# Kernel tuning notes

Measured on AMD Instinct MI355X. Metric: run time of the kernel, lower is better.

Reference implementation:

```python
import jax, jax.numpy as jnp
import numpy as np

H = 64          # hidden_size
L = 5           # num_layers
D_IN = 45       # input_size
D_LAT = 128     # latent dim
D_OUT = 4       # output classes


def _lstm_layer(x, W_ih, W_hh, b):
    """One LSTM layer, batch_first input x:[B,T,D]. PyTorch gate order i,f,g,o."""
    # Precompute input contribution for all timesteps: [B,T,4H]
    xg = jnp.einsum('btd,gd->btg', x, W_ih) + b
    xg = jnp.swapaxes(xg, 0, 1)  # [T,B,4H] for scan
    B = x.shape[0]
    h0 = jnp.zeros((B, H), x.dtype)
    c0 = jnp.zeros((B, H), x.dtype)

    def step(carry, xt):
        h, c = carry
        g = xt + h @ W_hh.T                      # [B,4H]
        i, f, gg, o = jnp.split(g, 4, axis=-1)
        c = jax.nn.sigmoid(f) * c + jax.nn.sigmoid(i) * jnp.tanh(gg)
        h = jax.nn.sigmoid(o) * jnp.tanh(c)
        return (h, c), h

    (_, _), hs = jax.lax.scan(step, (h0, c0), xg)  # hs: [T,B,H]
    return jnp.swapaxes(hs, 0, 1)                  # [B,T,H]


def setup_inputs() -> dict:
    key = jax.random.key(0)
    ks = jax.random.split(key, 12)
    s = 1.0 / np.sqrt(H)  # PyTorch LSTM init scale
    x = jax.random.normal(ks[0], (256, 2048, D_IN), jnp.float32)
    W_ih0 = jax.random.uniform(ks[1], (4 * H, D_IN), jnp.float32, -s, s)
    W_ih_rest = jax.random.uniform(ks[2], (L - 1, 4 * H, H), jnp.float32, -s, s)
    W_hh = jax.random.uniform(ks[3], (L, 4 * H, H), jnp.float32, -s, s)
    b_ih = jax.random.uniform(ks[4], (L, 4 * H), jnp.float32, -s, s)
    b_hh = jax.random.uniform(ks[5], (L, 4 * H), jnp.float32, -s, s)
    Wl = jax.random.normal(ks[6], (D_LAT, H), jnp.float32) * 0.05
    bl = jnp.zeros((D_LAT,), jnp.float32)
    Wo = jax.random.normal(ks[7], (D_OUT, D_LAT), jnp.float32) * 0.05
    bo = jnp.zeros((D_OUT,), jnp.float32)
    return dict(x=x, W_ih0=W_ih0, W_ih_rest=W_ih_rest, W_hh=W_hh,
                b_ih=b_ih, b_hh=b_hh, Wl=Wl, bl=bl, Wo=Wo, bo=bo)


def reference(x, W_ih0, W_ih_rest, W_hh, b_ih, b_hh, Wl, bl, Wo, bo):
    # 5-layer LSTM (eval mode: inter-layer dropout inactive)
    h = _lstm_layer(x, W_ih0, W_hh[0], b_ih[0] + b_hh[0])
    for l in range(1, L):
        h = _lstm_layer(h, W_ih_rest[l - 1], W_hh[l], b_ih[l] + b_hh[l])
    last = h[:, -1, :]                                  # [B,H]
    features = jax.nn.gelu(last @ Wl.T + bl, approximate=False)  # [B,128]
    out = jax.nn.relu(features @ Wo.T + bo)             # [B,4]
    return out, features
```

## Files before the change

### kernel.cpp

```cpp
#include <hip/hip_runtime.h>
#include <hip/hip_fp16.h>
#include <math.h>

#define NCH   1024
#define KMAX  1034
#define HID   64
typedef unsigned int uint;
typedef __attribute__((ext_vector_type(2))) _Float16 h2t;

__device__ __forceinline__ float sigmoid_(float x){ return 1.0f/(1.0f+__expf(-x)); }
__device__ __forceinline__ float tanh_(float x){ float e=__expf(2.0f*x); return 1.0f-2.0f/(e+1.0f); }

__device__ __forceinline__ float fdot2_(uint w, uint h, float acc){
#if __has_builtin(__builtin_amdgcn_fdot2)
    return __builtin_amdgcn_fdot2(__builtin_bit_cast(h2t,w), __builtin_bit_cast(h2t,h), acc, false);
#else
    __half2 wv = *reinterpret_cast<const __half2*>(&w);
    __half2 hv = *reinterpret_cast<const __half2*>(&h);
    float2 wf = __half22float2(wv), hf = __half22float2(hv);
    return fmaf(wf.x, hf.x, fmaf(wf.y, hf.y, acc));
#endif
}
__device__ __forceinline__ uint packh(float a, float b){
    uint ha = (uint)__half_as_ushort(__float2half(a));
    uint hb = (uint)__half_as_ushort(__float2half(b));
    return (hb<<16)|ha;
}
__device__ __forceinline__ uint4 pack8(const float* p){
    return make_uint4(packh(p[0],p[1]), packh(p[2],p[3]), packh(p[4],p[5]), packh(p[6],p[7]));
}

#define DOT4(A, W, H) do{ \
    A=fdot2_((W).x,(H).x,A); A=fdot2_((W).y,(H).y,A); \
    A=fdot2_((W).z,(H).z,A); A=fdot2_((W).w,(H).w,A); }while(0)

__global__ __attribute__((amdgpu_waves_per_eu(1,1))) __launch_bounds__(256)
void lstm_pipe4(const float* __restrict__ x,
                const float* __restrict__ W_ih0,
                const float* __restrict__ W_ih_rest,
                const float* __restrict__ W_hh,
                const float* __restrict__ b_ih,
                const float* __restrict__ b_hh,
                float* __restrict__ h_last)
{
    __shared__ float s_xg[2][5][2][256];
    __shared__ uint  s_wo [5][8][64][4];
    __shared__ uint  s_wih[10][8][64][4];
    __shared__ uint  s_hh[4][2][2][32];
    __shared__ uint  s_h16[5][32];
    __shared__ uint  s_x[2][2][24];

    const int tid  = threadIdx.x;
    const int wave = tid >> 6;
    const int lane = tid & 63;
    const int sm   = blockIdx.x;
    const float* x_s = x + (size_t)sm * 2048 * 45;
    float* hlast_g = h_last + (size_t)sm * HID;

    uint4 wU[48];
    float b0=0,b1=0,b2=0,b3=0,b4=0,b5=0,b6=0,b7=0,b8=0,b9=0;
    float cA=0.f, cB=0.f;

    if (wave == 0 || wave == 1){
#pragma unroll
        for (int li=0; li<2; ++li){
            const int L = wave*2 + li;
            const float* base = W_hh + (size_t)L*256*64;
#pragma unroll
            for (int d=0; d<8; ++d){
                wU[li*24 + 0*8 + d] = pack8(base + (size_t)(  0+lane)*64 + 8*d);
                wU[li*24 + 1*8 + d] = pack8(base + (size_t)( 64+lane)*64 + 8*d);
                wU[li*24 + 2*8 + d] = pack8(base + (size_t)(128+lane)*64 + 8*d);
                *(uint4*)&s_wo[L][d][lane][0] = pack8(base + (size_t)(192+lane)*64 + 8*d);
            }
            if (lane<32) s_h16[L][lane]=0u;
        }
#pragma unroll
        for (int g=0; g<2; ++g){
            const int row = wave*128 + g*64 + lane;
            const float* src = W_ih_rest + ((size_t)3*256 + row)*64;
            const int grp = 6 + wave*2 + g;
#pragma unroll
            for (int d=0; d<8; ++d)
                *(uint4*)&s_wih[grp][d][lane][0] = pack8(src + 8*d);
        }
        { int r0 = 4*256 + wave*128 + lane, r1 = r0 + 64;
          b0 = b_ih[r0]+b_hh[r0]; b1 = b_ih[r1]+b_hh[r1]; }
    } else if (wave == 2){
        const float* base = W_hh + (size_t)4*256*64;
#pragma unroll
        for (int d=0; d<8; ++d){
            wU[0*8+d] = pack8(base + (size_t)(  0+lane)*64 + 8*d);
            wU[1*8+d] = pack8(base + (size_t)( 64+lane)*64 + 8*d);
            wU[2*8+d] = pack8(base + (size_t)(128+lane)*64 + 8*d);
            *(uint4*)&s_wo[4][d][lane][0] = pack8(base + (size_t)(192+lane)*64 + 8*d);
        }
        if (lane<32) s_h16[4][lane]=0u;
#pragma unroll
        for (int g=0; g<4; ++g){
            const float* src = W_ih0 + (size_t)(g*64+lane)*45;
#pragma unroll
            for (int d=0; d<6; ++d){
                float e0=(8*d+0<45)?src[8*d+0]:0.f, e1=(8*d+1<45)?src[8*d+1]:0.f;
                float e2=(8*d+2<45)?src[8*d+2]:0.f, e3=(8*d+3<45)?src[8*d+3]:0.f;
                float e4=(8*d+4<45)?src[8*d+4]:0.f, e5=(8*d+5<45)?src[8*d+5]:0.f;
                float e6=(8*d+6<45)?src[8*d+6]:0.f, e7=(8*d+7<45)?src[8*d+7]:0.f;
                wU[24 + g*6 + d] = make_uint4(packh(e0,e1),packh(e2,e3),packh(e4,e5),packh(e6,e7));
            }
        }
        { int r;
          r=      lane; b0=b_ih[r]+b_hh[r];
          r=  64+lane;  b1=b_ih[r]+b_hh[r];
          r= 128+lane;  b2=b_ih[r]+b_hh[r];
          r= 192+lane;  b3=b_ih[r]+b_hh[r]; }
#pragma unroll
        for (int g=0; g<2; ++g){
            const int row = 128 + g*64 + lane;
            const float* src = W_ih_rest + ((size_t)1*256 + row)*64;
#pragma unroll
            for (int d=0; d<8; ++d)
                *(uint4*)&s_wih[g][d][lane][0] = pack8(src + 8*d);
        }
        { int r0=2*256+128+lane, r1=2*256+192+lane;
          b4=b_ih[r0]+b_hh[r0]; b5=b_ih[r1]+b_hh[r1]; }
        if (lane < 12){
            int bb=lane/6, t=(lane%6)/3, d=45+lane%3;
            ((__half*)&s_x[bb][t][0])[d]=__float2half(0.f);
        }
    } else {
#pragma unroll
        for (int g=0; g<6; ++g){
            const int ly  = (g<4) ? 1 : 2;
            const int row = (g<4) ? g*64+lane : (g-4)*64+lane;
            const float* src = W_ih_rest + ((size_t)(ly-1)*256 + row)*64;
#pragma unroll
            for (int d=0; d<8; ++d) wU[g*8+d] = pack8(src + 8*d);
        }
        { int r;
          r=1*256+  0+lane; b0=b_ih[r]+b_hh[r];
          r=1*256+ 64+lane; b1=b_ih[r]+b_hh[r];
          r=1*256+128+lane; b2=b_ih[r]+b_hh[r];
          r=1*256+192+lane; b3=b_ih[r]+b_hh[r];
          r=2*256+  0+lane; b4=b_ih[r]+b_hh[r];
          r=2*256+ 64+lane; b5=b_ih[r]+b_hh[r]; }
#pragma unroll
        for (int g=0; g<4; ++g){
            const float* src = W_ih_rest + ((size_t)2*256 + g*64+lane)*64;
#pragma unroll
            for (int d=0; d<8; ++d) *(uint4*)&s_wih[2+g][d][lane][0] = pack8(src + 8*d);
        }
        { int r;
          r=3*256+  0+lane; b6=b_ih[r]+b_hh[r];
          r=3*256+ 64+lane; b7=b_ih[r]+b_hh[r];
          r=3*256+128+lane; b8=b_ih[r]+b_hh[r];
          r=3*256+192+lane; b9=b_ih[r]+b_hh[r]; }
    }
    __syncthreads();

#define R_STEPN(L, WB, LASTF, T, C, CST) do{                                   \
    const int buf_ = (C)&1;                                                    \
    float xi_ = s_xg[buf_][L][T][      lane];                                  \
    float xf_ = s_xg[buf_][L][T][ 64 + lane];                                  \
    float xgg_= s_xg[buf_][L][T][128 + lane];                                  \
    float xo_ = s_xg[buf_][L][T][192 + lane];                                  \
    float ai0=0,ai1=0, af0=0,af1=0, ag0=0,ag1=0, ao0=0,ao1=0;                  \
    _Pragma("unroll")                                                          \
    for (int d_=0; d_<8; d_+=2){                                               \
        uint4 h0_ = *(const uint4*)&s_h16[L][4*d_];                            \
        uint4 h1_ = *(const uint4*)&s_h16[L][4*d_+4];                          \
        uint4 woA_ = *(const uint4*)&s_wo[L][d_  ][lane][0];                   \
        uint4 woB_ = *(const uint4*)&s_wo[L][d_+1][lane][0];                   \
        DOT4(ai0, wU[(WB)+d_],      h0_); DOT4(ai1, wU[(WB)+d_+1],    h1_);    \
        DOT4(af0, wU[(WB)+8+d_],    h0_); DOT4(af1, wU[(WB)+8+d_+1],  h1_);    \
        DOT4(ag0, wU[(WB)+16+d_],   h0_); DOT4(ag1, wU[(WB)+16+d_+1], h1_);    \
        DOT4(ao0, woA_,             h0_); DOT4(ao1, woB_,             h1_);    \
    }                                                                          \
    float I_=sigmoid_(xi_+(ai0+ai1)), F_=sigmoid_(xf_+(af0+af1));              \
    float G_=tanh_(xgg_+(ag0+ag1)),   O_=sigmoid_(xo_+(ao0+ao1));              \
    CST = fmaf(F_, CST, I_*G_);                                                \
    float h_ = O_*tanh_(CST);                                                  \
    __half hhi_=__float2half(h_);                                              \
    ((__half*)&s_h16[L][0])[lane]=hhi_;                                        \
    if (!(LASTF)){                                                             \
        ((__half*)&s_hh[(L)<4?(L):0][buf_][T][0])[lane]=hhi_;                  \
    } else if ((C)==NCH-1 && (T)==1){ hlast_g[lane]=h_; }                      \
}while(0)

#define G4T(DMAX, WEXPR, H0, H1, XD0, XD1, B0_,B1_,B2_,B3_) do{                \
    float a00=(B0_),a01=(B1_),a02=(B2_),a03=(B3_);                             \
    float a10=(B0_),a11=(B1_),a12=(B2_),a13=(B3_);                             \
    _Pragma("unroll")                                                          \
    for (int d_=0; d_<(DMAX); ++d_){                                           \
        uint4 w0_=WEXPR(0,d_), w1_=WEXPR(1,d_), w2_=WEXPR(2,d_), w3_=WEXPR(3,d_);\
        uint4 h0_=*(const uint4*)&(H0)[4*d_];                                  \
        uint4 h1_=*(const uint4*)&(H1)[4*d_];                                  \
        DOT4(a00,w0_,h0_); DOT4(a01,w1_,h0_); DOT4(a02,w2_,h0_); DOT4(a03,w3_,h0_);\
        DOT4(a10,w0_,h1_); DOT4(a11,w1_,h1_); DOT4(a12,w2_,h1_); DOT4(a13,w3_,h1_);\
    }                                                                          \
    (XD0)[      lane]=a00; (XD0)[ 64+lane]=a01;                                \
    (XD0)[128+lane]=a02;   (XD0)[192+lane]=a03;                                \
    (XD1)[      lane]=a10; (XD1)[ 64+lane]=a11;                                \
    (XD1)[128+lane]=a12;   (XD1)[192+lane]=a13;                                \
}while(0)

#define G2T(DMAX, WEXPR, H0, H1, XD0, XD1, ROWOFF, B0_,B1_) do{                \
    float a00=(B0_),a01=(B1_), a10=(B0_),a11=(B1_);                            \
    _Pragma("unroll")                                                          \
    for (int d_=0; d_<(DMAX); ++d_){                                           \
        uint4 wa_ = WEXPR(0,d_), wb_ = WEXPR(1,d_);                            \
        uint4 h0_=*(const uint4*)&(H0)[4*d_];                                  \
        uint4 h1_=*(const uint4*)&(H1)[4*d_];                                  \
        DOT4(a00,wa_,h0_); DOT4(a01,wb_,h0_);                                  \
        DOT4(a10,wa_,h1_); DOT4(a11,wb_,h1_);                                  \
    }                                                                          \
    (XD0)[(ROWOFF)+lane]=a00; (XD0)[(ROWOFF)+64+lane]=a01;                     \
    (XD1)[(ROWOFF)+lane]=a10; (XD1)[(ROWOFF)+64+lane]=a11;                     \
}while(0)

#define W_L1(g,d)  wU[(g)*8+(d)]
#define W_L2R(g,d) wU[32+(g)*8+(d)]
#define W_L0(g,d)  wU[24+(g)*6+(d)]
#define W_L2L(g,d) (*(const uint4*)&s_wih[(g)][d][lane][0])
#define W_L3(g,d)  (*(const uint4*)&s_wih[2+(g)][d][lane][0])
#define W_L4A(g,d) (*(const uint4*)&s_wih[6+(g)][d][lane][0])
#define W_L4B(g,d) (*(const uint4*)&s_wih[8+(g)][d][lane][0])

#define STAGE_X() do{                                                          \
    const int bufx = k & 1;                                                    \
    _Pragma("unroll")                                                          \
    for (int r=0; r<2; ++r){                                                   \
        const int i = lane + 64*r;                                             \
        if (i < 90){                                                           \
            float v = x_s[(size_t)k*90 + i];                                   \
            const int t = i/45, d = i - 45*t;                                  \
            ((__half*)&s_x[bufx][t][0])[d] = __float2half(v);                  \
        }                                                                      \
    }                                                                          \
}while(0)

#define BODY_W0(GUARDED) do{                                                   \
    const int c0=k-2, c1=k-4, cl=k-9;                                          \
    if (!(GUARDED) || (c0>=0 && c0<NCH)){                                      \
        R_STEPN(0,  0, 0, 0, c0, cA); }                                        \
    if (!(GUARDED) || (c1>=0 && c1<NCH)){                                      \
        R_STEPN(1, 24, 0, 0, c1, cB); }                                        \
    if (!(GUARDED) || (c0>=0 && c0<NCH)){                                      \
        R_STEPN(0,  0, 0, 1, c0, cA); }                                        \
    if (!(GUARDED) || (c1>=0 && c1<NCH)){                                      \
        R_STEPN(1, 24, 0, 1, c1, cB); }                                        \
    if (!(GUARDED) || (cl>=0 && cl<NCH)){                                      \
        const int bl=cl&1;                                                     \
        G2T(8, W_L4A, (&s_hh[3][bl][0][0]), (&s_hh[3][bl][1][0]),              \
            (&s_xg[bl][4][0][0]), (&s_xg[bl][4][1][0]), 0, b0,b1); }           \
}while(0)

#define BODY_W1(GUARDED) do{                                                   \
    const int c2=k-6, c3=k-8, cl=k-9;                                          \
    if (!(GUARDED) || (c2>=0 && c2<NCH)){                                      \
        R_STEPN(2,  0, 0, 0, c2, cA); }                                        \
    if (!(GUARDED) || (c3>=0 && c3<NCH)){                                      \
        R_STEPN(3, 24, 0, 0, c3, cB); }                                        \
    if (!(GUARDED) || (c2>=0 && c2<NCH)){                                      \
        R_STEPN(2,  0, 0, 1, c2, cA); }                                        \
    if (!(GUARDED) || (c3>=0 && c3<NCH)){                                      \
        R_STEPN(3, 24, 0, 1, c3, cB); }                                        \
    if (!(GUARDED) || (cl>=0 && cl<NCH)){                                      \
        const int bl=cl&1;                                                     \
        G2T(8, W_L4B, (&s_hh[3][bl][0][0]), (&s_hh[3][bl][1][0]),              \
            (&s_xg[bl][4][0][0]), (&s_xg[bl][4][1][0]), 128, b0,b1); }         \
}while(0)

#define BODY_W2(GUARDED) do{                                                   \
    if (!(GUARDED) || (k < NCH)) STAGE_X();                                    \
    const int c4=k-10, cg0=k-1, cg2=k-5;                                       \
    if (!(GUARDED) || (c4>=0 && c4<NCH)){                                      \
        R_STEPN(4, 0, 1, 0, c4, cA); }                                         \
    if (!(GUARDED) || (cg0>=0 && cg0<NCH)){                                    \
        const int bg=cg0&1;                                                    \
        G4T(6, W_L0, (&s_x[bg][0][0]), (&s_x[bg][1][0]),                       \
            (&s_xg[bg][0][0][0]), (&s_xg[bg][0][1][0]), b0,b1,b2,b3); }        \
    if (!(GUARDED) || (c4>=0 && c4<NCH)){                                      \
        R_STEPN(4, 0, 1, 1, c4, cA); }                                         \
    if (!(GUARDED) || (cg2>=0 && cg2<NCH)){                                    \
        const int bg=cg2&1;                                                    \
        G2T(8, W_L2L, (&s_hh[1][bg][0][0]), (&s_hh[1][bg][1][0]),              \
            (&s_xg[bg][2][0][0]), (&s_xg[bg][2][1][0]), 128, b4,b5); }         \
}while(0)

#define BODY_W3(GUARDED) do{                                                   \
    const int cg1=k-3, cg2=k-5, cg3=k-7;                                       \
    if (!(GUARDED) || (cg1>=0 && cg1<NCH)){                                    \
        const int bg=cg1&1;                                                    \
        G4T(8, W_L1, (&s_hh[0][bg][0][0]), (&s_hh[0][bg][1][0]),               \
            (&s_xg[bg][1][0][0]), (&s_xg[bg][1][1][0]), b0,b1,b2,b3); }        \
    if (!(GUARDED) || (cg2>=0 && cg2<NCH)){                                    \
        const int bg=cg2&1;                                                    \
        G2T(8, W_L2R, (&s_hh[1][bg][0][0]), (&s_hh[1][bg][1][0]),              \
            (&s_xg[bg][2][0][0]), (&s_xg[bg][2][1][0]), 0, b4,b5); }           \
    if (!(GUARDED) || (cg3>=0 && cg3<NCH)){                                    \
        const int bg=cg3&1;                                                    \
        G4T(8, W_L3, (&s_hh[2][bg][0][0]), (&s_hh[2][bg][1][0]),               \
            (&s_xg[bg][3][0][0]), (&s_xg[bg][3][1][0]), b6,b7,b8,b9); }        \
}while(0)

    for (int k=0; k<KMAX; ++k){
        if (k >= 10 && k < NCH){
            if      (wave == 0) BODY_W0(0);
            else if (wave == 1) BODY_W1(0);
            else if (wave == 2) BODY_W2(0);
            else                BODY_W3(0);
        } else {
            if      (wave == 0) BODY_W0(1);
            else if (wave == 1) BODY_W1(1);
            else if (wave == 2) BODY_W2(1);
            else                BODY_W3(1);
        }
        __syncthreads();
    }
}

__global__ __launch_bounds__(128)
void head_kernel(const float* __restrict__ h_last,
                 const float* __restrict__ Wl,
                 const float* __restrict__ bl,
                 const float* __restrict__ Wo,
                 const float* __restrict__ bo,
                 float* __restrict__ d_out)
{
    __shared__ float s_last[HID];
    __shared__ float s_feat[128];
    const int s = blockIdx.x;
    const int j = threadIdx.x;

    if (j < HID) s_last[j] = h_last[(size_t)s * HID + j];
    __syncthreads();

    float acc = bl[j];
#pragma unroll
    for (int k = 0; k < HID; ++k)
        acc = fmaf(s_last[k], Wl[j * HID + k], acc);
    float f = 0.5f * acc * (1.0f + erff(acc * 0.70710678118654752440f));
    d_out[256 * 4 + s * 128 + j] = f;
    s_feat[j] = f;
    __syncthreads();

    if (j < 4) {
        float a = bo[j];
#pragma unroll
        for (int k = 0; k < 128; ++k)
            a = fmaf(s_feat[k], Wo[j * 128 + k], a);
        d_out[s * 4 + j] = fmaxf(a, 0.0f);
    }
}

extern "C" void kernel_launch(void* const* d_in, const int* in_sizes, int n_in,
                              void* d_out, int out_size, void* d_ws, size_t ws_size,
                              hipStream_t stream)
{
    const float* x         = (const float*)d_in[0];
    const float* W_ih0     = (const float*)d_in[1];
    const float* W_ih_rest = (const float*)d_in[2];
    const float* W_hh      = (const float*)d_in[3];
    const float* b_ih      = (const float*)d_in[4];
    const float* b_hh      = (const float*)d_in[5];
    const float* Wl        = (const float*)d_in[6];
    const float* bl        = (const float*)d_in[7];
    const float* Wo        = (const float*)d_in[8];
    const float* bo        = (const float*)d_in[9];

    float* h_last = (float*)d_ws;

    lstm_pipe4<<<256, 256, 0, stream>>>(
        x, W_ih0, W_ih_rest, W_hh, b_ih, b_hh, h_last);
    head_kernel<<<256, 128, 0, stream>>>(h_last, Wl, bl, Wo, bo, (float*)d_out);
}
```

Measured before the change: 4.621 ms.

## Stream packed recurrent weights from global memory instead of LDS

Adds a small pre-pass kernel that converts the output-gate recurrent weights and some input weights to packed fp16 and writes them to workspace. The main kernel drops those large shared arrays and reads the packed weights from global memory (through the cache) inside the recurrent step and the gate GEMV macros. This removes per-block packing work and shared-memory staging, but puts global or L2 loads on the latency-critical serial recurrence path. The launch also requests 61440 bytes of dynamic shared memory that the kernel does not appear to use.

New measurement: 17.10 ms. +270.1%, slower.

```diff
diff --git a/kernel.cpp b/kernel.cpp
--- a/kernel.cpp
+++ b/kernel.cpp
@@ -34,6 +34,28 @@
     A=fdot2_((W).x,(H).x,A); A=fdot2_((W).y,(H).y,A); \
     A=fdot2_((W).z,(H).z,A); A=fdot2_((W).w,(H).w,A); }while(0)
 
+__global__ __launch_bounds__(256)
+void pack_weights(const float* __restrict__ W_ih_rest,
+                  const float* __restrict__ W_hh,
+                  uint4* __restrict__ gWo,
+                  uint4* __restrict__ gWih)
+{
+    const int idx = blockIdx.x * 256 + threadIdx.x;
+    if (idx >= 7680) return;
+    if (idx < 2560){
+        const int lane = idx & 63, d = (idx >> 6) & 7, L = idx >> 9;
+        gWo[idx] = pack8(W_hh + (size_t)L*256*64 + (size_t)(192+lane)*64 + 8*d);
+    } else {
+        const int j = idx - 2560;
+        const int lane = j & 63, d = (j >> 6) & 7, grp = j >> 9;
+        int ly, row;
+        if (grp < 2){ ly = 1; row = 128 + grp*64 + lane; }
+        else if (grp < 6){ ly = 2; row = (grp-2)*64 + lane; }
+        else { ly = 3; row = (grp-6)*64 + lane; }
+        gWih[j] = pack8(W_ih_rest + ((size_t)ly*256 + row)*64 + 8*d);
+    }
+}
+
 __global__ __attribute__((amdgpu_waves_per_eu(1,1))) __launch_bounds__(256)
 void lstm_pipe4(const float* __restrict__ x,
                 const float* __restrict__ W_ih0,
@@ -41,11 +63,11 @@
                 const float* __restrict__ W_hh,
                 const float* __restrict__ b_ih,
                 const float* __restrict__ b_hh,
+                const uint4* __restrict__ gWo,
+                const uint4* __restrict__ gWih,
                 float* __restrict__ h_last)
 {
     __shared__ float s_xg[2][5][2][256];
-    __shared__ uint  s_wo [5][8][64][4];
-    __shared__ uint  s_wih[10][8][64][4];
     __shared__ uint  s_hh[4][2][2][32];
     __shared__ uint  s_h16[5][32];
     __shared__ uint  s_x[2][2][24];
@@ -71,18 +93,8 @@
                 wU[li*24 + 0*8 + d] = pack8(base + (size_t)(  0+lane)*64 + 8*d);
                 wU[li*24 + 1*8 + d] = pack8(base + (size_t)( 64+lane)*64 + 8*d);
                 wU[li*24 + 2*8 + d] = pack8(base + (size_t)(128+lane)*64 + 8*d);
-                *(uint4*)&s_wo[L][d][lane][0] = pack8(base + (size_t)(192+lane)*64 + 8*d);
             }
             if (lane<32) s_h16[L][lane]=0u;
-        }
-#pragma unroll
-        for (int g=0; g<2; ++g){
-            const int row = wave*128 + g*64 + lane;
-            const float* src = W_ih_rest + ((size_t)3*256 + row)*64;
-            const int grp = 6 + wave*2 + g;
-#pragma unroll
-            for (int d=0; d<8; ++d)
-                *(uint4*)&s_wih[grp][d][lane][0] = pack8(src + 8*d);
         }
         { int r0 = 4*256 + wave*128 + lane, r1 = r0 + 64;
           b0 = b_ih[r0]+b_hh[r0]; b1 = b_ih[r1]+b_hh[r1]; }
@@ -93,7 +105,6 @@
             wU[0*8+d] = pack8(base + (size_t)(  0+lane)*64 + 8*d);
             wU[1*8+d] = pack8(base + (size_t)( 64+lane)*64 + 8*d);
             wU[2*8+d] = pack8(base + (size_t)(128+lane)*64 + 8*d);
-            *(uint4*)&s_wo[4][d][lane][0] = pack8(base + (size_t)(192+lane)*64 + 8*d);
         }
         if (lane<32) s_h16[4][lane]=0u;
 #pragma unroll
@@ -113,14 +124,6 @@
           r=  64+lane;  b1=b_ih[r]+b_hh[r];
           r= 128+lane;  b2=b_ih[r]+b_hh[r];
           r= 192+lane;  b3=b_ih[r]+b_hh[r]; }
-#pragma unroll
-        for (int g=0; g<2; ++g){
-            const int row = 128 + g*64 + lane;
-            const float* src = W_ih_rest + ((size_t)1*256 + row)*64;
-#pragma unroll
-            for (int d=0; d<8; ++d)
-                *(uint4*)&s_wih[g][d][lane][0] = pack8(src + 8*d);
-        }
         { int r0=2*256+128+lane, r1=2*256+192+lane;
           b4=b_ih[r0]+b_hh[r0]; b5=b_ih[r1]+b_hh[r1]; }
         if (lane < 12){
@@ -142,14 +145,7 @@
           r=1*256+128+lane; b2=b_ih[r]+b_hh[r];
           r=1*256+192+lane; b3=b_ih[r]+b_hh[r];
           r=2*256+  0+lane; b4=b_ih[r]+b_hh[r];
-          r=2*256+ 64+lane; b5=b_ih[r]+b_hh[r]; }
-#pragma unroll
-        for (int g=0; g<4; ++g){
-            const float* src = W_ih_rest + ((size_t)2*256 + g*64+lane)*64;
-#pragma unroll
-            for (int d=0; d<8; ++d) *(uint4*)&s_wih[2+g][d][lane][0] = pack8(src + 8*d);
-        }
-        { int r;
+          r=2*256+ 64+lane; b5=b_ih[r]+b_hh[r];
           r=3*256+  0+lane; b6=b_ih[r]+b_hh[r];
           r=3*256+ 64+lane; b7=b_ih[r]+b_hh[r];
           r=3*256+128+lane; b8=b_ih[r]+b_hh[r];
@@ -168,8 +164,8 @@
     for (int d_=0; d_<8; d_+=2){                                               \
         uint4 h0_ = *(const uint4*)&s_h16[L][4*d_];                            \
         uint4 h1_ = *(const uint4*)&s_h16[L][4*d_+4];                          \
-        uint4 woA_ = *(const uint4*)&s_wo[L][d_  ][lane][0];                   \
-        uint4 woB_ = *(const uint4*)&s_wo[L][d_+1][lane][0];                   \
+        uint4 woA_ = gWo[((L)*8 + d_    )*64 + lane];                          \
+        uint4 woB_ = gWo[((L)*8 + d_ + 1)*64 + lane];                          \
         DOT4(ai0, wU[(WB)+d_],      h0_); DOT4(ai1, wU[(WB)+d_+1],    h1_);    \
         DOT4(af0, wU[(WB)+8+d_],    h0_); DOT4(af1, wU[(WB)+8+d_+1],  h1_);    \
         DOT4(ag0, wU[(WB)+16+d_],   h0_); DOT4(ag1, wU[(WB)+16+d_+1], h1_);    \
@@ -220,10 +216,10 @@
 #define W_L1(g,d)  wU[(g)*8+(d)]
 #define W_L2R(g,d) wU[32+(g)*8+(d)]
 #define W_L0(g,d)  wU[24+(g)*6+(d)]
-#define W_L2L(g,d) (*(const uint4*)&s_wih[(g)][d][lane][0])
-#define W_L3(g,d)  (*(const uint4*)&s_wih[2+(g)][d][lane][0])
-#define W_L4A(g,d) (*(const uint4*)&s_wih[6+(g)][d][lane][0])
-#define W_L4B(g,d) (*(const uint4*)&s_wih[8+(g)][d][lane][0])
+#define W_L2L(g,d) (gWih[(((g)    )*8+(d))*64 + lane])
+#define W_L3(g,d)  (gWih[((2+(g))*8+(d))*64 + lane])
+#define W_L4A(g,d) (gWih[((6+(g))*8+(d))*64 + lane])
+#define W_L4B(g,d) (gWih[((8+(g))*8+(d))*64 + lane])
 
 #define STAGE_X() do{                                                          \
     const int bufx = k & 1;                                                    \
@@ -240,14 +236,10 @@
 
 #define BODY_W0(GUARDED) do{                                                   \
     const int c0=k-2, c1=k-4, cl=k-9;                                          \
-    if (!(GUARDED) || (c0>=0 && c0<NCH)){                                      \
-        R_STEPN(0,  0, 0, 0, c0, cA); }                                        \
-    if (!(GUARDED) || (c1>=0 && c1<NCH)){                                      \
-        R_STEPN(1, 24, 0, 0, c1, cB); }                                        \
-    if (!(GUARDED) || (c0>=0 && c0<NCH)){                                      \
-        R_STEPN(0,  0, 0, 1, c0, cA); }                                        \
-    if (!(GUARDED) || (c1>=0 && c1<NCH)){                                      \
-        R_STEPN(1, 24, 0, 1, c1, cB); }                                        \
+    if (!(GUARDED) || (c0>=0 && c0<NCH)){ R_STEPN(0,  0, 0, 0, c0, cA); }      \
+    if (!(GUARDED) || (c1>=0 && c1<NCH)){ R_STEPN(1, 24, 0, 0, c1, cB); }      \
+    if (!(GUARDED) || (c0>=0 && c0<NCH)){ R_STEPN(0,  0, 0, 1, c0, cA); }      \
+    if (!(GUARDED) || (c1>=0 && c1<NCH)){ R_STEPN(1, 24, 0, 1, c1, cB); }      \
     if (!(GUARDED) || (cl>=0 && cl<NCH)){                                      \
         const int bl=cl&1;                                                     \
         G2T(8, W_L4A, (&s_hh[3][bl][0][0]), (&s_hh[3][bl][1][0]),              \
@@ -256,14 +248,10 @@
 
 #define BODY_W1(GUARDED) do{                                                   \
     const int c2=k-6, c3=k-8, cl=k-9;                                          \
-    if (!(GUARDED) || (c2>=0 && c2<NCH)){                                      \
-        R_STEPN(2,  0, 0, 0, c2, cA); }                                        \
-    if (!(GUARDED) || (c3>=0 && c3<NCH)){                                      \
-        R_STEPN(3, 24, 0, 0, c3, cB); }                                        \
-    if (!(GUARDED) || (c2>=0 && c2<NCH)){                                      \
-        R_STEPN(2,  0, 0, 1, c2, cA); }                                        \
-    if (!(GUARDED) || (c3>=0 && c3<NCH)){                                      \
-        R_STEPN(3, 24, 0, 1, c3, cB); }                                        \
+    if (!(GUARDED) || (c2>=0 && c2<NCH)){ R_STEPN(2,  0, 0, 0, c2, cA); }      \
+    if (!(GUARDED) || (c3>=0 && c3<NCH)){ R_STEPN(3, 24, 0, 0, c3, cB); }      \
+    if (!(GUARDED) || (c2>=0 && c2<NCH)){ R_STEPN(2,  0, 0, 1, c2, cA); }      \
+    if (!(GUARDED) || (c3>=0 && c3<NCH)){ R_STEPN(3, 24, 0, 1, c3, cB); }      \
     if (!(GUARDED) || (cl>=0 && cl<NCH)){                                      \
         const int bl=cl&1;                                                     \
         G2T(8, W_L4B, (&s_hh[3][bl][0][0]), (&s_hh[3][bl][1][0]),              \
@@ -273,14 +261,12 @@
 #define BODY_W2(GUARDED) do{                                                   \
     if (!(GUARDED) || (k < NCH)) STAGE_X();                                    \
     const int c4=k-10, cg0=k-1, cg2=k-5;                                       \
-    if (!(GUARDED) || (c4>=0 && c4<NCH)){                                      \
-        R_STEPN(4, 0, 1, 0, c4, cA); }                                         \
+    if (!(GUARDED) || (c4>=0 && c4<NCH)){ R_STEPN(4, 0, 1, 0, c4, cA); }       \
     if (!(GUARDED) || (cg0>=0 && cg0<NCH)){                                    \
         const int bg=cg0&1;                                                    \
         G4T(6, W_L0, (&s_x[bg][0][0]), (&s_x[bg][1][0]),                       \
             (&s_xg[bg][0][0][0]), (&s_xg[bg][0][1][0]), b0,b1,b2,b3); }        \
-    if (!(GUARDED) || (c4>=0 && c4<NCH)){                                      \
-        R_STEPN(4, 0, 1, 1, c4, cA); }                                         \
+    if (!(GUARDED) || (c4>=0 && c4<NCH)){ R_STEPN(4, 0, 1, 1, c4, cA); }       \
     if (!(GUARDED) || (cg2>=0 && cg2<NCH)){                                    \
         const int bg=cg2&1;                                                    \
         G2T(8, W_L2L, (&s_hh[1][bg][0][0]), (&s_hh[1][bg][1][0]),              \
@@ -369,8 +355,11 @@
     const float* bo        = (const float*)d_in[9];
 
     float* h_last = (float*)d_ws;
-
-    lstm_pipe4<<<256, 256, 0, stream>>>(
-        x, W_ih0, W_ih_rest, W_hh, b_ih, b_hh, h_last);
+    uint4* gWo  = (uint4*)((char*)d_ws + 65536);
+    uint4* gWih = (uint4*)((char*)d_ws + 65536 + 40960);
+
+    pack_weights<<<30, 256, 0, stream>>>(W_ih_rest, W_hh, gWo, gWih);
+    lstm_pipe4<<<256, 256, 61440, stream>>>(
+        x, W_ih0, W_ih_rest, W_hh, b_ih, b_hh, gWo, gWih, h_last);
     head_kernel<<<256, 128, 0, stream>>>(h_last, Wl, bl, Wo, bo, (float*)d_out);
 }
```

## Process four timesteps per pipeline chunk and store gate preactivations in half

Applied to the files above, without the earlier changes.

Each pipeline stage now handles four timesteps per chunk instead of two, which halves the number of chunks and therefore the number of block-wide barriers. The input-projection GEMV macros are restructured to reuse each weight load across four timesteps. The staged gate preactivations (s_xg) are now stored as fp16 so the larger buffers still fit in shared memory. The cost is lower precision on the preactivations, and in the recurrent waves the serial work per barrier interval roughly doubles, which may change load balance between waves.

Result: slower. 14.46 ms (+212.8%).

```diff
diff --git a/kernel.cpp b/kernel.cpp
--- a/kernel.cpp
+++ b/kernel.cpp
@@ -2,8 +2,9 @@
 #include <hip/hip_fp16.h>
 #include <math.h>
 
-#define NCH   1024
-#define KMAX  1034
+#define CH    4
+#define NCH   512
+#define KMAX  522
 #define HID   64
 typedef unsigned int uint;
 typedef __attribute__((ext_vector_type(2))) _Float16 h2t;
@@ -43,12 +44,12 @@
                 const float* __restrict__ b_hh,
                 float* __restrict__ h_last)
 {
-    __shared__ float s_xg[2][5][2][256];
+    __shared__ __half s_xg[2][5][CH][256];
     __shared__ uint  s_wo [5][8][64][4];
     __shared__ uint  s_wih[10][8][64][4];
-    __shared__ uint  s_hh[4][2][2][32];
+    __shared__ uint  s_hh[4][2][CH][32];
     __shared__ uint  s_h16[5][32];
-    __shared__ uint  s_x[2][2][24];
+    __shared__ uint  s_x[2][CH][24];
 
     const int tid  = threadIdx.x;
     const int wave = tid >> 6;
@@ -123,8 +124,8 @@
         }
         { int r0=2*256+128+lane, r1=2*256+192+lane;
           b4=b_ih[r0]+b_hh[r0]; b5=b_ih[r1]+b_hh[r1]; }
-        if (lane < 12){
-            int bb=lane/6, t=(lane%6)/3, d=45+lane%3;
+        if (lane < 2*CH*3){
+            int bb=lane/(CH*3), rem=lane%(CH*3), t=rem/3, d=45+rem%3;
             ((__half*)&s_x[bb][t][0])[d]=__float2half(0.f);
         }
     } else {
@@ -159,10 +160,10 @@
 
 #define R_STEPN(L, WB, LASTF, T, C, CST) do{                                   \
     const int buf_ = (C)&1;                                                    \
-    float xi_ = s_xg[buf_][L][T][      lane];                                  \
-    float xf_ = s_xg[buf_][L][T][ 64 + lane];                                  \
-    float xgg_= s_xg[buf_][L][T][128 + lane];                                  \
-    float xo_ = s_xg[buf_][L][T][192 + lane];                                  \
+    float xi_ = __half2float(s_xg[buf_][L][T][      lane]);                    \
+    float xf_ = __half2float(s_xg[buf_][L][T][ 64 + lane]);                    \
+    float xgg_= __half2float(s_xg[buf_][L][T][128 + lane]);                    \
+    float xo_ = __half2float(s_xg[buf_][L][T][192 + lane]);                    \
     float ai0=0,ai1=0, af0=0,af1=0, ag0=0,ag1=0, ao0=0,ao1=0;                  \
     _Pragma("unroll")                                                          \
     for (int d_=0; d_<8; d_+=2){                                               \
@@ -183,55 +184,51 @@
     ((__half*)&s_h16[L][0])[lane]=hhi_;                                        \
     if (!(LASTF)){                                                             \
         ((__half*)&s_hh[(L)<4?(L):0][buf_][T][0])[lane]=hhi_;                  \
-    } else if ((C)==NCH-1 && (T)==1){ hlast_g[lane]=h_; }                      \
-}while(0)
-
-#define G4T(DMAX, WEXPR, H0, H1, XD0, XD1, B0_,B1_,B2_,B3_) do{                \
-    float a00=(B0_),a01=(B1_),a02=(B2_),a03=(B3_);                             \
-    float a10=(B0_),a11=(B1_),a12=(B2_),a13=(B3_);                             \
-    _Pragma("unroll")                                                          \
-    for (int d_=0; d_<(DMAX); ++d_){                                           \
-        uint4 w0_=WEXPR(0,d_), w1_=WEXPR(1,d_), w2_=WEXPR(2,d_), w3_=WEXPR(3,d_);\
-        uint4 h0_=*(const uint4*)&(H0)[4*d_];                                  \
-        uint4 h1_=*(const uint4*)&(H1)[4*d_];                                  \
-        DOT4(a00,w0_,h0_); DOT4(a01,w1_,h0_); DOT4(a02,w2_,h0_); DOT4(a03,w3_,h0_);\
-        DOT4(a10,w0_,h1_); DOT4(a11,w1_,h1_); DOT4(a12,w2_,h1_); DOT4(a13,w3_,h1_);\
-    }                                                                          \
-    (XD0)[      lane]=a00; (XD0)[ 64+lane]=a01;                                \
-    (XD0)[128+lane]=a02;   (XD0)[192+lane]=a03;                                \
-    (XD1)[      lane]=a10; (XD1)[ 64+lane]=a11;                                \
-    (XD1)[128+lane]=a12;   (XD1)[192+lane]=a13;                                \
-}while(0)
-
-#define G2T(DMAX, WEXPR, H0, H1, XD0, XD1, ROWOFF, B0_,B1_) do{                \
-    float a00=(B0_),a01=(B1_), a10=(B0_),a11=(B1_);                            \
+    } else if ((C)==NCH-1 && (T)==CH-1){ hlast_g[lane]=h_; }                   \
+}while(0)
+
+#define G2Q(DMAX, WEXPR, HB, HSTR, XB, ROWOFF, B0_,B1_) do{                    \
+    float a00=(B0_),a01=(B0_),a02=(B0_),a03=(B0_);                             \
+    float a10=(B1_),a11=(B1_),a12=(B1_),a13=(B1_);                             \
     _Pragma("unroll")                                                          \
     for (int d_=0; d_<(DMAX); ++d_){                                           \
         uint4 wa_ = WEXPR(0,d_), wb_ = WEXPR(1,d_);                            \
-        uint4 h0_=*(const uint4*)&(H0)[4*d_];                                  \
-        uint4 h1_=*(const uint4*)&(H1)[4*d_];                                  \
-        DOT4(a00,wa_,h0_); DOT4(a01,wb_,h0_);                                  \
-        DOT4(a10,wa_,h1_); DOT4(a11,wb_,h1_);                                  \
+        uint4 h0_=*(const uint4*)&(HB)[0*(HSTR)+4*d_];                         \
+        uint4 h1_=*(const uint4*)&(HB)[1*(HSTR)+4*d_];                         \
+        uint4 h2_=*(const uint4*)&(HB)[2*(HSTR)+4*d_];                         \
+        uint4 h3_=*(const uint4*)&(HB)[3*(HSTR)+4*d_];                         \
+        DOT4(a00,wa_,h0_); DOT4(a01,wa_,h1_); DOT4(a02,wa_,h2_); DOT4(a03,wa_,h3_);\
+        DOT4(a10,wb_,h0_); DOT4(a11,wb_,h1_); DOT4(a12,wb_,h2_); DOT4(a13,wb_,h3_);\
     }                                                                          \
-    (XD0)[(ROWOFF)+lane]=a00; (XD0)[(ROWOFF)+64+lane]=a01;                     \
-    (XD1)[(ROWOFF)+lane]=a10; (XD1)[(ROWOFF)+64+lane]=a11;                     \
-}while(0)
-
-#define W_L1(g,d)  wU[(g)*8+(d)]
+    __half* xp_ = (__half*)(XB);                                               \
+    xp_[0*256+(ROWOFF)+lane]=__float2half(a00);                                \
+    xp_[1*256+(ROWOFF)+lane]=__float2half(a01);                                \
+    xp_[2*256+(ROWOFF)+lane]=__float2half(a02);                                \
+    xp_[3*256+(ROWOFF)+lane]=__float2half(a03);                                \
+    xp_[0*256+(ROWOFF)+64+lane]=__float2half(a10);                             \
+    xp_[1*256+(ROWOFF)+64+lane]=__float2half(a11);                             \
+    xp_[2*256+(ROWOFF)+64+lane]=__float2half(a12);                             \
+    xp_[3*256+(ROWOFF)+64+lane]=__float2half(a13);                             \
+}while(0)
+
+#define W_L1A(g,d) wU[(g)*8+(d)]
+#define W_L1B(g,d) wU[(2+(g))*8+(d)]
 #define W_L2R(g,d) wU[32+(g)*8+(d)]
-#define W_L0(g,d)  wU[24+(g)*6+(d)]
+#define W_L0A(g,d) wU[24+(g)*6+(d)]
+#define W_L0B(g,d) wU[24+(2+(g))*6+(d)]
 #define W_L2L(g,d) (*(const uint4*)&s_wih[(g)][d][lane][0])
-#define W_L3(g,d)  (*(const uint4*)&s_wih[2+(g)][d][lane][0])
+#define W_L3A(g,d) (*(const uint4*)&s_wih[2+(g)][d][lane][0])
+#define W_L3B(g,d) (*(const uint4*)&s_wih[4+(g)][d][lane][0])
 #define W_L4A(g,d) (*(const uint4*)&s_wih[6+(g)][d][lane][0])
 #define W_L4B(g,d) (*(const uint4*)&s_wih[8+(g)][d][lane][0])
 
 #define STAGE_X() do{                                                          \
     const int bufx = k & 1;                                                    \
     _Pragma("unroll")                                                          \
-    for (int r=0; r<2; ++r){                                                   \
+    for (int r=0; r<3; ++r){                                                   \
         const int i = lane + 64*r;                                             \
-        if (i < 90){                                                           \
-            float v = x_s[(size_t)k*90 + i];                                   \
+        if (i < CH*45){                                                        \
+            float v = x_s[(size_t)k*(CH*45) + i];                              \
             const int t = i/45, d = i - 45*t;                                  \
             ((__half*)&s_x[bufx][t][0])[d] = __float2half(v);                  \
         }                                                                      \
@@ -240,67 +237,75 @@
 
 #define BODY_W0(GUARDED) do{                                                   \
     const int c0=k-2, c1=k-4, cl=k-9;                                          \
-    if (!(GUARDED) || (c0>=0 && c0<NCH)){                                      \
-        R_STEPN(0,  0, 0, 0, c0, cA); }                                        \
-    if (!(GUARDED) || (c1>=0 && c1<NCH)){                                      \
-        R_STEPN(1, 24, 0, 0, c1, cB); }                                        \
-    if (!(GUARDED) || (c0>=0 && c0<NCH)){                                      \
-        R_STEPN(0,  0, 0, 1, c0, cA); }                                        \
-    if (!(GUARDED) || (c1>=0 && c1<NCH)){                                      \
-        R_STEPN(1, 24, 0, 1, c1, cB); }                                        \
+    if (!(GUARDED) || (c0>=0 && c0<NCH)){ R_STEPN(0,  0, 0, 0, c0, cA); }      \
+    if (!(GUARDED) || (c1>=0 && c1<NCH)){ R_STEPN(1, 24, 0, 0, c1, cB); }      \
+    if (!(GUARDED) || (c0>=0 && c0<NCH)){ R_STEPN(0,  0, 0, 1, c0, cA); }      \
+    if (!(GUARDED) || (c1>=0 && c1<NCH)){ R_STEPN(1, 24, 0, 1, c1, cB); }      \
+    if (!(GUARDED) || (c0>=0 && c0<NCH)){ R_STEPN(0,  0, 0, 2, c0, cA); }      \
+    if (!(GUARDED) || (c1>=0 && c1<NCH)){ R_STEPN(1, 24, 0, 2, c1, cB); }      \
+    if (!(GUARDED) || (c0>=0 && c0<NCH)){ R_STEPN(0,  0, 0, 3, c0, cA); }      \
+    if (!(GUARDED) || (c1>=0 && c1<NCH)){ R_STEPN(1, 24, 0, 3, c1, cB); }      \
     if (!(GUARDED) || (cl>=0 && cl<NCH)){                                      \
         const int bl=cl&1;                                                     \
-        G2T(8, W_L4A, (&s_hh[3][bl][0][0]), (&s_hh[3][bl][1][0]),              \
-            (&s_xg[bl][4][0][0]), (&s_xg[bl][4][1][0]), 0, b0,b1); }           \
+        G2Q(8, W_L4A, (&s_hh[3][bl][0][0]), 32,                                \
+            (&s_xg[bl][4][0][0]), 0, b0,b1); }                                 \
 }while(0)
 
 #define BODY_W1(GUARDED) do{                                                   \
     const int c2=k-6, c3=k-8, cl=k-9;                                          \
-    if (!(GUARDED) || (c2>=0 && c2<NCH)){                                      \
-        R_STEPN(2,  0, 0, 0, c2, cA); }                                        \
-    if (!(GUARDED) || (c3>=0 && c3<NCH)){                                      \
-        R_STEPN(3, 24, 0, 0, c3, cB); }                                        \
-    if (!(GUARDED) || (c2>=0 && c2<NCH)){                                      \
-        R_STEPN(2,  0, 0, 1, c2, cA); }                                        \
-    if (!(GUARDED) || (c3>=0 && c3<NCH)){                                      \
-        R_STEPN(3, 24, 0, 1, c3, cB); }                                        \
+    if (!(GUARDED) || (c2>=0 && c2<NCH)){ R_STEPN(2,  0, 0, 0, c2, cA); }      \
+    if (!(GUARDED) || (c3>=0 && c3<NCH)){ R_STEPN(3, 24, 0, 0, c3, cB); }      \
+    if (!(GUARDED) || (c2>=0 && c2<NCH)){ R_STEPN(2,  0, 0, 1, c2, cA); }      \
+    if (!(GUARDED) || (c3>=0 && c3<NCH)){ R_STEPN(3, 24, 0, 1, c3, cB); }      \
+    if (!(GUARDED) || (c2>=0 && c2<NCH)){ R_STEPN(2,  0, 0, 2, c2, cA); }      \
+    if (!(GUARDED) || (c3>=0 && c3<NCH)){ R_STEPN(3, 24, 0, 2, c3, cB); }      \
+    if (!(GUARDED) || (c2>=0 && c2<NCH)){ R_STEPN(2,  0, 0, 3, c2, cA); }      \
+    if (!(GUARDED) || (c3>=0 && c3<NCH)){ R_STEPN(3, 24, 0, 3, c3, cB); }      \
     if (!(GUARDED) || (cl>=0 && cl<NCH)){                                      \
         const int bl=cl&1;                                                     \
-        G2T(8, W_L4B, (&s_hh[3][bl][0][0]), (&s_hh[3][bl][1][0]),              \
-            (&s_xg[bl][4][0][0]), (&s_xg[bl][4][1][0]), 128, b0,b1); }         \
+        G2Q(8, W_L4B, (&s_hh[3][bl][0][0]), 32,                                \
+            (&s_xg[bl][4][0][0]), 128, b0,b1); }                               \
 }while(0)
 
 #define BODY_W2(GUARDED) do{                                                   \
     if (!(GUARDED) || (k < NCH)) STAGE_X();                                    \
     const int c4=k-10, cg0=k-1, cg2=k-5;                                       \
-    if (!(GUARDED) || (c4>=0 && c4<NCH)){                                      \
-        R_STEPN(4, 0, 1, 0, c4, cA); }                                         \
+    if (!(GUARDED) || (c4>=0 && c4<NCH)){ R_STEPN(4, 0, 1, 0, c4, cA); }       \
+    if (!(GUARDED) || (c4>=0 && c4<NCH)){ R_STEPN(4, 0, 1, 1, c4, cA); }       \
     if (!(GUARDED) || (cg0>=0 && cg0<NCH)){                                    \
         const int bg=cg0&1;                                                    \
-        G4T(6, W_L0, (&s_x[bg][0][0]), (&s_x[bg][1][0]),                       \
-            (&s_xg[bg][0][0][0]), (&s_xg[bg][0][1][0]), b0,b1,b2,b3); }        \
-    if (!(GUARDED) || (c4>=0 && c4<NCH)){                                      \
-        R_STEPN(4, 0, 1, 1, c4, cA); }                                         \
+        G2Q(6, W_L0A, (&s_x[bg][0][0]), 24,                                    \
+            (&s_xg[bg][0][0][0]), 0, b0,b1); }                                 \
+    if (!(GUARDED) || (c4>=0 && c4<NCH)){ R_STEPN(4, 0, 1, 2, c4, cA); }       \
+    if (!(GUARDED) || (c4>=0 && c4<NCH)){ R_STEPN(4, 0, 1, 3, c4, cA); }       \
+    if (!(GUARDED) || (cg0>=0 && cg0<NCH)){                                    \
+        const int bg=cg0&1;                                                    \
+        G2Q(6, W_L0B, (&s_x[bg][0][0]), 24,                                    \
+            (&s_xg[bg][0][0][0]), 128, b2,b3); }                               \
     if (!(GUARDED) || (cg2>=0 && cg2<NCH)){                                    \
         const int bg=cg2&1;                                                    \
-        G2T(8, W_L2L, (&s_hh[1][bg][0][0]), (&s_hh[1][bg][1][0]),              \
-            (&s_xg[bg][2][0][0]), (&s_xg[bg][2][1][0]), 128, b4,b5); }         \
+        G2Q(8, W_L2L, (&s_hh[1][bg][0][0]), 32,                                \
+            (&s_xg[bg][2][0][0]), 128, b4,b5); }                               \
 }while(0)
 
 #define BODY_W3(GUARDED) do{                                                   \
     const int cg1=k-3, cg2=k-5, cg3=k-7;                                       \
     if (!(GUARDED) || (cg1>=0 && cg1<NCH)){                                    \
         const int bg=cg1&1;                                                    \
-        G4T(8, W_L1, (&s_hh[0][bg][0][0]), (&s_hh[0][bg][1][0]),               \
-            (&s_xg[bg][1][0][0]), (&s_xg[bg][1][1][0]), b0,b1,b2,b3); }        \
+        G2Q(8, W_L1A, (&s_hh[0][bg][0][0]), 32,                                \
+            (&s_xg[bg][1][0][0]), 0, b0,b1);                                   \
+        G2Q(8, W_L1B, (&s_hh[0][bg][0][0]), 32,                                \
+            (&s_xg[bg][1][0][0]), 128, b2,b3); }                               \
     if (!(GUARDED) || (cg2>=0 && cg2<NCH)){                                    \
         const int bg=cg2&1;                                                    \
-        G2T(8, W_L2R, (&s_hh[1][bg][0][0]), (&s_hh[1][bg][1][0]),              \
-            (&s_xg[bg][2][0][0]), (&s_xg[bg][2][1][0]), 0, b4,b5); }           \
+        G2Q(8, W_L2R, (&s_hh[1][bg][0][0]), 32,                                \
+            (&s_xg[bg][2][0][0]), 0, b4,b5); }                                 \
     if (!(GUARDED) || (cg3>=0 && cg3<NCH)){                                    \
         const int bg=cg3&1;                                                    \
-        G4T(8, W_L3, (&s_hh[2][bg][0][0]), (&s_hh[2][bg][1][0]),               \
-            (&s_xg[bg][3][0][0]), (&s_xg[bg][3][1][0]), b6,b7,b8,b9); }        \
+        G2Q(8, W_L3A, (&s_hh[2][bg][0][0]), 32,                                \
+            (&s_xg[bg][3][0][0]), 0, b6,b7);                                   \
+        G2Q(8, W_L3B, (&s_hh[2][bg][0][0]), 32,                                \
+            (&s_xg[bg][3][0][0]), 128, b8,b9); }                               \
 }while(0)
 
     for (int k=0; k<KMAX; ++k){
```
